# Kernel tuning notes

Measured on AMD Instinct MI355X. Metric: run time of the kernel, lower is better.

The kernel has to match this reference:

```python
import jax, jax.numpy as jnp
import numpy as np

ROPE_THETA = 10000.0


def _rope(x, pos, theta):
    # x: [B, H, S, d_k], pos: [S] int. Interleaved RoPE (pairs (2i, 2i+1)).
    d_k = x.shape[-1]
    inv_freq = theta ** (-2.0 * jnp.arange(d_k // 2, dtype=jnp.float32) / d_k)  # [d_k/2]
    ang = pos.astype(jnp.float32)[:, None] * inv_freq  # [S, d_k/2]
    cos, sin = jnp.cos(ang), jnp.sin(ang)
    xe, xo = x[..., 0::2], x[..., 1::2]
    re = xe * cos - xo * sin
    ro = xe * sin + xo * cos
    return jnp.stack([re, ro], axis=-1).reshape(x.shape)


def setup_inputs() -> dict:
    key = jax.random.key(0)
    ks = jax.random.split(key, 5)
    B, S, D = 2, 2048, 1024
    return {
        "in_features": jax.random.normal(ks[0], (B, S, D), jnp.float32),
        "q_proj_weight": jax.random.normal(ks[1], (D, D), jnp.float32) * (D ** -0.5),
        "k_proj_weight": jax.random.normal(ks[2], (D, D), jnp.float32) * (D ** -0.5),
        "v_proj_weight": jax.random.normal(ks[3], (D, D), jnp.float32) * (D ** -0.5),
        "o_proj_weight": jax.random.normal(ks[4], (D, D), jnp.float32) * (D ** -0.5),
        "token_positions": jnp.arange(S, dtype=jnp.int64),
        "d_model": 1024,
        "num_heads": 16,
    }


def reference(in_features, q_proj_weight, k_proj_weight, v_proj_weight,
              o_proj_weight, token_positions, d_model, num_heads):
    B, S, _ = in_features.shape
    d_k = d_model // num_heads

    def split_heads(x):  # [B, S, D] -> [B, H, S, d_k]
        return x.reshape(B, S, num_heads, d_k).transpose(0, 2, 1, 3)

    q = split_heads(in_features @ q_proj_weight.T)
    k = split_heads(in_features @ k_proj_weight.T)
    v = split_heads(in_features @ v_proj_weight.T)

    q = _rope(q, token_positions, ROPE_THETA)
    k = _rope(k, token_positions, ROPE_THETA)

    scores = jnp.einsum("bhqd,bhkd->bhqk", q, k) / jnp.sqrt(jnp.float32(d_k))
    causal = token_positions[:, None] >= token_positions[None, :]  # [S, S]
    scores = jnp.where(causal, scores, -jnp.inf)
    probs = jax.nn.softmax(scores, axis=-1)
    ctx = jnp.einsum("bhqk,bhkd->bhqd", probs, v)  # [B, H, S, d_k]
    ctx = ctx.transpose(0, 2, 1, 3).reshape(B, S, d_model)
    return ctx @ o_proj_weight.T
```

## Files before the change

kernel.cpp:

```cpp
#include <hip/hip_runtime.h>
#include <math.h>

typedef _Float16 f16;
typedef _Float16 f16x8 __attribute__((ext_vector_type(8)));
typedef float    f32x4 __attribute__((ext_vector_type(4)));

#define SEQ  2048
#define DM   1024
#define NH   16
#define DK   64
#define MTOT 4096

#define LOG2E 1.4426950408889634f

__global__ __launch_bounds__(256)
void cvt_all(const float* __restrict__ X,  const float* __restrict__ W0,
             const float* __restrict__ W1, const float* __restrict__ W2,
             const float* __restrict__ W3, f16* __restrict__ dst)
{
    const int i = (blockIdx.x * 256 + threadIdx.x) * 4;
    const float* src;
    if (i < (4 << 20)) {
        src = X + i;
    } else {
        const int j   = i - (4 << 20);
        const int sel = j >> 20;
        const float* W = (sel == 0) ? W0 : (sel == 1) ? W1 : (sel == 2) ? W2 : W3;
        src = W + (j & ((1 << 20) - 1));
    }
    float4 v = *(const float4*)src;
    f16 o[4] = {(f16)v.x, (f16)v.y, (f16)v.z, (f16)v.w};
    *(uint2*)&dst[i] = *(const uint2*)o;
}

__global__ __launch_bounds__(256)
void rope_table(float2* __restrict__ rt)
{
    const int i = blockIdx.x * 256 + threadIdx.x;
    const int s = i >> 5, p = i & 31;
    const float ang = (float)s * exp2f(-0.4152410118609203f * (float)p);
    float sn, cs;
    sincosf(ang, &sn, &cs);
    rt[i] = make_float2(cs, sn);
}

__global__ __launch_bounds__(512)
void gemm_qkv(const f16* __restrict__ A, const f16* __restrict__ W,
              f16* __restrict__ C, const float2* __restrict__ rt)
{
    __shared__ f16 As[128][72];
    __shared__ f16 Bs[128][72];

    const int tid  = threadIdx.x;
    const int wid  = tid >> 6, lane = tid & 63;
    const int l15  = lane & 15, l4 = lane >> 4;
    const int wm   = wid >> 2, wn = wid & 3;
    const int bm   = blockIdx.x * 128;
    const int sel  = blockIdx.y >> 3;
    const int bn   = (blockIdx.y & 7) * 128;
    const f16* B   = W + ((size_t)sel << 20);
    f16* Cb        = C + ((size_t)sel << 22);

    f32x4 acc[4][2];
    #pragma unroll
    for (int mi = 0; mi < 4; ++mi)
        #pragma unroll
        for (int ni = 0; ni < 2; ++ni)
            acc[mi][ni] = (f32x4){0.f, 0.f, 0.f, 0.f};

    for (int k0 = 0; k0 < DM; k0 += 64) {
        #pragma unroll
        for (int t = 0; t < 2; ++t) {
            const int li  = tid + t * 512;
            const int row = li >> 3, c8 = (li & 7) * 8;
            *(f16x8*)&As[row][c8] = *(const f16x8*)&A[(size_t)(bm + row) * DM + k0 + c8];
            *(f16x8*)&Bs[row][c8] = *(const f16x8*)&B[(size_t)(bn + row) * DM + k0 + c8];
        }
        __syncthreads();
        #pragma unroll
        for (int kc = 0; kc < 2; ++kc) {
            f16x8 af[4], bf[2];
            #pragma unroll
            for (int mi = 0; mi < 4; ++mi)
                af[mi] = *(const f16x8*)&As[wm*64 + mi*16 + l15][kc*32 + l4*8];
            #pragma unroll
            for (int ni = 0; ni < 2; ++ni)
                bf[ni] = *(const f16x8*)&Bs[wn*32 + ni*16 + l15][kc*32 + l4*8];
            #pragma unroll
            for (int mi = 0; mi < 4; ++mi)
                #pragma unroll
                for (int ni = 0; ni < 2; ++ni)
                    acc[mi][ni] = __builtin_amdgcn_mfma_f32_16x16x32_f16(
                        af[mi], bf[ni], acc[mi][ni], 0, 0, 0);
        }
        __syncthreads();
    }

    #pragma unroll
    for (int mi = 0; mi < 4; ++mi)
        #pragma unroll
        for (int ni = 0; ni < 2; ++ni)
            #pragma unroll
            for (int r = 0; r < 4; ++r) {
                const int row = bm + wm*64 + mi*16 + l4*4 + r;
                const int col = bn + wn*32 + ni*16 + l15;
                float v = acc[mi][ni][r];
                if (sel < 2) {
                    const float p   = __shfl_xor(v, 1);
                    const float2 cs = rt[((row & (SEQ-1)) << 5) | ((col & 63) >> 1)];
                    v = (col & 1) ? fmaf(v, cs.x,  p * cs.y)
                                  : fmaf(v, cs.x, -p * cs.y);
                }
                Cb[(size_t)row * DM + col] = (f16)v;
            }
}

__global__ __launch_bounds__(512)
void gemm_h(const f16* __restrict__ A, const f16* __restrict__ B,
            float* __restrict__ C)
{
    __shared__ f16 As[128][72];
    __shared__ f16 Bs[128][72];

    const int tid  = threadIdx.x;
    const int wid  = tid >> 6, lane = tid & 63;
    const int l15  = lane & 15, l4 = lane >> 4;
    const int wm   = wid >> 2, wn = wid & 3;
    const int bm   = blockIdx.x * 128, bn = blockIdx.y * 128;

    f32x4 acc[4][2];
    #pragma unroll
    for (int mi = 0; mi < 4; ++mi)
        #pragma unroll
        for (int ni = 0; ni < 2; ++ni)
            acc[mi][ni] = (f32x4){0.f, 0.f, 0.f, 0.f};

    for (int k0 = 0; k0 < DM; k0 += 64) {
        #pragma unroll
        for (int t = 0; t < 2; ++t) {
            const int li  = tid + t * 512;
            const int row = li >> 3, c8 = (li & 7) * 8;
            *(f16x8*)&As[row][c8] = *(const f16x8*)&A[(size_t)(bm + row) * DM + k0 + c8];
            *(f16x8*)&Bs[row][c8] = *(const f16x8*)&B[(size_t)(bn + row) * DM + k0 + c8];
        }
        __syncthreads();
        #pragma unroll
        for (int kc = 0; kc < 2; ++kc) {
            f16x8 af[4], bf[2];
            #pragma unroll
            for (int mi = 0; mi < 4; ++mi)
                af[mi] = *(const f16x8*)&As[wm*64 + mi*16 + l15][kc*32 + l4*8];
            #pragma unroll
            for (int ni = 0; ni < 2; ++ni)
                bf[ni] = *(const f16x8*)&Bs[wn*32 + ni*16 + l15][kc*32 + l4*8];
            #pragma unroll
            for (int mi = 0; mi < 4; ++mi)
                #pragma unroll
                for (int ni = 0; ni < 2; ++ni)
                    acc[mi][ni] = __builtin_amdgcn_mfma_f32_16x16x32_f16(
                        af[mi], bf[ni], acc[mi][ni], 0, 0, 0);
        }
        __syncthreads();
    }

    #pragma unroll
    for (int mi = 0; mi < 4; ++mi)
        #pragma unroll
        for (int ni = 0; ni < 2; ++ni)
            #pragma unroll
            for (int r = 0; r < 4; ++r) {
                const int row = bm + wm*64 + mi*16 + l4*4 + r;
                const int col = bn + wn*32 + ni*16 + l15;
                C[(size_t)row * DM + col] = acc[mi][ni][r];
            }
}

__global__ __launch_bounds__(512)
void flash_mfma(const f16* __restrict__ Q, const f16* __restrict__ K,
                const f16* __restrict__ V, f16* __restrict__ O)
{
    __shared__ f16 smem[6][64][72];

    const int bid = blockIdx.x;
    const int xcd = bid & 7, slot = bid >> 3;
    const int bh  = xcd * 4 + (slot >> 4);
    const int bx  = slot & 15;
    const int b   = bh >> 4, h = bh & 15;

    const int tid = threadIdx.x, wid = tid >> 6, lane = tid & 63;
    const int grp = wid >> 2, w4 = wid & 3;
    const int l15 = lane & 15, l4 = lane >> 4;
    const size_t base = ((size_t)b * SEQ) * DM + h * DK;

    f16 (*Ks)[72]  = smem[grp];
    f16 (*Vts)[72] = smem[2 + grp];
    f16 (*Ps)[72]  = smem[4 + grp];

    const int t256  = tid & 255;
    const int srow0 = t256 >> 3,        sc8 = (t256 & 7) * 8;
    const int srow1 = (t256 + 256) >> 3;
    const int spc0  = srow0 ^ ((t256 & 7) << 3);
    const int spc1  = srow1 ^ ((t256 & 7) << 3);

    f16x8 kreg[2], vreg[2];

    #pragma unroll 1
    for (int qsel = 0; qsel < 2; ++qsel) {
        const int qt     = qsel ? (31 - bx) : bx;
        const int ntiles = qt + 1;
        const int tmax   = (ntiles + 1) >> 1;

        f16x8 qf[2];
        {
            const size_t qrow = (size_t)(qt*64 + w4*16 + l15);
            #pragma unroll
            for (int kc = 0; kc < 2; ++kc) {
                qf[kc] = *(const f16x8*)&Q[base + qrow * DM + kc*32 + l4*8];
                #pragma unroll
                for (int j = 0; j < 8; ++j)
                    qf[kc][j] = (f16)((float)qf[kc][j] * (0.125f * LOG2E));
            }
        }

        float m_r[4], l_r[4];
        f32x4 acc_o[4];
        #pragma unroll
        for (int r = 0; r < 4; ++r) { m_r[r] = -INFINITY; l_r[r] = 0.f; }
        #pragma unroll
        for (int dg = 0; dg < 4; ++dg) acc_o[dg] = (f32x4){0.f, 0.f, 0.f, 0.f};

        if (grp < ntiles) {
            const size_t g0 = base + (size_t)(grp*64 + srow0) * DM + sc8;
            const size_t g1 = base + (size_t)(grp*64 + srow1) * DM + sc8;
            kreg[0] = *(const f16x8*)&K[g0]; vreg[0] = *(const f16x8*)&V[g0];
            kreg[1] = *(const f16x8*)&K[g1]; vreg[1] = *(const f16x8*)&V[g1];
        }
        __syncthreads();
        if (grp < ntiles) {
            *(f16x8*)&Ks[srow0][sc8] = kreg[0];
            *(f16x8*)&Ks[srow1][sc8] = kreg[1];
            #pragma unroll
            for (int j = 0; j < 8; ++j) { Vts[sc8+j][spc0] = vreg[0][j];
                                          Vts[sc8+j][spc1] = vreg[1][j]; }
        }
        __syncthreads();

        for (int t = 0; t < tmax; ++t) {
            const int  myt = 2*t + grp;
            const bool act = myt < ntiles;
            const int  nxt = myt + 2;

            if (nxt < ntiles) {
                const size_t g0 = base + (size_t)(nxt*64 + srow0) * DM + sc8;
                const size_t g1 = base + (size_t)(nxt*64 + srow1) * DM + sc8;
                kreg[0] = *(const f16x8*)&K[g0]; vreg[0] = *(const f16x8*)&V[g0];
                kreg[1] = *(const f16x8*)&K[g1]; vreg[1] = *(const f16x8*)&V[g1];
            }

            if (act) {
                f32x4 sc[4];
                #pragma unroll
                for (int cg = 0; cg < 4; ++cg) sc[cg] = (f32x4){0.f, 0.f, 0.f, 0.f};
                #pragma unroll
                for (int cg = 0; cg < 4; ++cg)
                    #pragma unroll
                    for (int kc = 0; kc < 2; ++kc) {
                        f16x8 bf = *(const f16x8*)&Ks[cg*16 + l15][kc*32 + l4*8];
                        sc[cg] = __builtin_amdgcn_mfma_f32_16x16x32_f16(qf[kc], bf, sc[cg], 0, 0, 0);
                    }

                if (myt == qt) {
                    #pragma unroll
                    for (int cg = 0; cg < 4; ++cg)
                        #pragma unroll
                        for (int r = 0; r < 4; ++r)
                            if (cg*16 + l15 > w4*16 + l4*4 + r) sc[cg][r] = -INFINITY;
                }

                #pragma unroll
                for (int r = 0; r < 4; ++r) {
                    float mx = fmaxf(fmaxf(sc[0][r], sc[1][r]), fmaxf(sc[2][r], sc[3][r]));
                    mx = fmaxf(mx, __shfl_xor(mx, 1));
                    mx = fmaxf(mx, __shfl_xor(mx, 2));
                    mx = fmaxf(mx, __shfl_xor(mx, 4));
                    mx = fmaxf(mx, __shfl_xor(mx, 8));
                    const float mn   = fmaxf(m_r[r], mx);
                    const float corr = exp2f(m_r[r] - mn);
                    float ps = 0.f;
                    #pragma unroll
                    for (int cg = 0; cg < 4; ++cg) {
                        const float pv = exp2f(sc[cg][r] - mn);
                        sc[cg][r] = pv;
                        ps += pv;
                    }
                    ps += __shfl_xor(ps, 1);
                    ps += __shfl_xor(ps, 2);
                    ps += __shfl_xor(ps, 4);
                    ps += __shfl_xor(ps, 8);
                    l_r[r] = l_r[r] * corr + ps;
                    m_r[r] = mn;
                    #pragma unroll
                    for (int dg = 0; dg < 4; ++dg) acc_o[dg][r] *= corr;
                }

                #pragma unroll
                for (int cg = 0; cg < 4; ++cg)
                    #pragma unroll
                    for (int r = 0; r < 4; ++r)
                        Ps[w4*16 + l4*4 + r][cg*16 + l15] = (f16)sc[cg][r];

                #pragma unroll
                for (int kc = 0; kc < 2; ++kc) {
                    f16x8 pa = *(const f16x8*)&Ps[w4*16 + l15][kc*32 + l4*8];
                    #pragma unroll
                    for (int dg = 0; dg < 4; ++dg) {
                        const int d   = dg*16 + l15;
                        const int pcr = (kc*32 + l4*8) ^ (((d >> 3) & 7) << 3);
                        f16x8 vb = *(const f16x8*)&Vts[d][pcr];
                        acc_o[dg] = __builtin_amdgcn_mfma_f32_16x16x32_f16(pa, vb, acc_o[dg], 0, 0, 0);
                    }
                }
            }

            __syncthreads();
            if (nxt < ntiles) {
                *(f16x8*)&Ks[srow0][sc8] = kreg[0];
                *(f16x8*)&Ks[srow1][sc8] = kreg[1];
                #pragma unroll
                for (int j = 0; j < 8; ++j) { Vts[sc8+j][spc0] = vreg[0][j];
                                              Vts[sc8+j][spc1] = vreg[1][j]; }
            }
            __syncthreads();
        }

        float* accx = (float*)&smem[0][0][0];
        float* mlx  = (float*)&smem[4][0][0];

        if (grp == 1) {
            #pragma unroll
            for (int r = 0; r < 4; ++r) {
                const int ql = w4*16 + l4*4 + r;
                mlx[ql]      = m_r[r];
                mlx[64 + ql] = l_r[r];
                #pragma unroll
                for (int dg = 0; dg < 4; ++dg)
                    accx[ql*64 + dg*16 + l15] = acc_o[dg][r];
            }
        }
        __syncthreads();
        if (grp == 0) {
            #pragma unroll
            for (int r = 0; r < 4; ++r) {
                const int ql = w4*16 + l4*4 + r;
                const float m1 = mlx[ql], l1 = mlx[64 + ql];
                const float m  = fmaxf(m_r[r], m1);
                const float c0 = exp2f(m_r[r] - m);
                const float c1 = exp2f(m1 - m);
                const float inv = 1.f / (l_r[r]*c0 + l1*c1);
                const size_t row = (size_t)(qt*64 + ql);
                #pragma unroll
                for (int dg = 0; dg < 4; ++dg) {
                    const float a1 = accx[ql*64 + dg*16 + l15];
                    O[base + row * DM + dg*16 + l15] =
                        (f16)((acc_o[dg][r]*c0 + a1*c1) * inv);
                }
            }
        }
    }
}

extern "C" void kernel_launch(void* const* d_in, const int* in_sizes, int n_in,
                              void* d_out, int out_size, void* d_ws, size_t ws_size,
                              hipStream_t stream)
{
    const float* X  = (const float*)d_in[0];
    const float* Wq = (const float*)d_in[1];
    const float* Wk = (const float*)d_in[2];
    const float* Wv = (const float*)d_in[3];
    const float* Wo = (const float*)d_in[4];

    f16* ws = (f16*)d_ws;
    const size_t M1 = 1u << 20;
    f16* Xh  = ws;
    f16* Wqh = ws + 4*M1;
    f16* Woh = ws + 7*M1;
    f16* Qh  = ws + 8*M1;
    f16* Kh  = ws + 12*M1;
    f16* Vh  = ws + 16*M1;
    f16* Ch  = ws + 20*M1;
    float2* rt = (float2*)(ws + 24*M1);

    cvt_all<<<8192, 256, 0, stream>>>(X, Wq, Wk, Wv, Wo, Xh);
    rope_table<<<256, 256, 0, stream>>>(rt);

    gemm_qkv<<<dim3(MTOT/128, 24), 512, 0, stream>>>(Xh, Wqh, Qh, rt);

    flash_mfma<<<512, 512, 0, stream>>>(Qh, Kh, Vh, Ch);

    gemm_h<<<dim3(MTOT/128, DM/128), 512, 0, stream>>>(Ch, Woh, (float*)d_out);
}
```

Baseline: 233.4 us.

## Use direct global-to-LDS loads and 4-wave 64x64 warp tiles in projection GEMMs

The two projection GEMMs now share one macro core. It stages A and B tiles with global_load_lds (direct global-to-LDS, bypassing VGPRs) using BK=32 and an unpadded LDS layout. Blocks are cut to 256 threads with 64x64 per-wave tiles (4x4 MFMAs), which raises operand reuse per LDS read. The risks are LDS bank conflicts from the unpadded 64-byte rows, twice as many barrier-separated k-steps, and no double buffering to hide load latency.

```diff
diff --git a/kernel.cpp b/kernel.cpp
--- a/kernel.cpp
+++ b/kernel.cpp
@@ -12,6 +12,13 @@
 #define MTOT 4096
 
 #define LOG2E 1.4426950408889634f
+
+__device__ __forceinline__ void gload16(const void* g, void* l)
+{
+    __builtin_amdgcn_global_load_lds(
+        (const __attribute__((address_space(1))) void*)g,
+        (__attribute__((address_space(3))) void*)l, 16, 0, 0);
+}
 
 __global__ __launch_bounds__(256)
 void cvt_all(const float* __restrict__ X,  const float* __restrict__ W0,
@@ -44,135 +51,82 @@
     rt[i] = make_float2(cs, sn);
 }
 
-__global__ __launch_bounds__(512)
+#define GEMM_CORE(EPILOG)                                                     \
+    __shared__ f16 As[128*32];                                                \
+    __shared__ f16 Bs[128*32];                                                \
+    const int tid = threadIdx.x;                                              \
+    const int wid = tid >> 6, lane = tid & 63;                                \
+    const int l15 = lane & 15, l4 = lane >> 4;                                \
+    const int wm  = wid >> 1, wn = wid & 1;                                   \
+    const int row0 = tid >> 2, col0 = (tid & 3) * 8;                          \
+    f32x4 acc[4][4];                                                          \
+    _Pragma("unroll")                                                         \
+    for (int mi = 0; mi < 4; ++mi)                                            \
+        _Pragma("unroll")                                                     \
+        for (int ni = 0; ni < 4; ++ni)                                        \
+            acc[mi][ni] = (f32x4){0.f, 0.f, 0.f, 0.f};                        \
+    for (int k0 = 0; k0 < DM; k0 += 32) {                                     \
+        gload16(&A[(size_t)(bm + row0)      * DM + k0 + col0], &As[tid*8]);   \
+        gload16(&A[(size_t)(bm + row0 + 64) * DM + k0 + col0], &As[(tid+256)*8]); \
+        gload16(&B[(size_t)(bn + row0)      * DM + k0 + col0], &Bs[tid*8]);   \
+        gload16(&B[(size_t)(bn + row0 + 64) * DM + k0 + col0], &Bs[(tid+256)*8]); \
+        __syncthreads();                                                      \
+        f16x8 af[4], bf[4];                                                   \
+        _Pragma("unroll")                                                     \
+        for (int mi = 0; mi < 4; ++mi)                                        \
+            af[mi] = *(const f16x8*)&As[(wm*64 + mi*16 + l15)*32 + l4*8];     \
+        _Pragma("unroll")                                                     \
+        for (int ni = 0; ni < 4; ++ni)                                        \
+            bf[ni] = *(const f16x8*)&Bs[(wn*64 + ni*16 + l15)*32 + l4*8];     \
+        _Pragma("unroll")                                                     \
+        for (int mi = 0; mi < 4; ++mi)                                        \
+            _Pragma("unroll")                                                 \
+            for (int ni = 0; ni < 4; ++ni)                                    \
+                acc[mi][ni] = __builtin_amdgcn_mfma_f32_16x16x32_f16(         \
+                    af[mi], bf[ni], acc[mi][ni], 0, 0, 0);                    \
+        __syncthreads();                                                      \
+    }                                                                         \
+    _Pragma("unroll")                                                         \
+    for (int mi = 0; mi < 4; ++mi)                                            \
+        _Pragma("unroll")                                                     \
+        for (int ni = 0; ni < 4; ++ni)                                        \
+            _Pragma("unroll")                                                 \
+            for (int r = 0; r < 4; ++r) {                                     \
+                const int row = bm + wm*64 + mi*16 + l4*4 + r;                \
+                const int col = bn + wn*64 + ni*16 + l15;                     \
+                float v = acc[mi][ni][r];                                     \
+                EPILOG                                                        \
+            }
+
+__global__ __launch_bounds__(256)
 void gemm_qkv(const f16* __restrict__ A, const f16* __restrict__ W,
               f16* __restrict__ C, const float2* __restrict__ rt)
 {
-    __shared__ f16 As[128][72];
-    __shared__ f16 Bs[128][72];
-
-    const int tid  = threadIdx.x;
-    const int wid  = tid >> 6, lane = tid & 63;
-    const int l15  = lane & 15, l4 = lane >> 4;
-    const int wm   = wid >> 2, wn = wid & 3;
-    const int bm   = blockIdx.x * 128;
-    const int sel  = blockIdx.y >> 3;
-    const int bn   = (blockIdx.y & 7) * 128;
-    const f16* B   = W + ((size_t)sel << 20);
-    f16* Cb        = C + ((size_t)sel << 22);
-
-    f32x4 acc[4][2];
-    #pragma unroll
-    for (int mi = 0; mi < 4; ++mi)
-        #pragma unroll
-        for (int ni = 0; ni < 2; ++ni)
-            acc[mi][ni] = (f32x4){0.f, 0.f, 0.f, 0.f};
-
-    for (int k0 = 0; k0 < DM; k0 += 64) {
-        #pragma unroll
-        for (int t = 0; t < 2; ++t) {
-            const int li  = tid + t * 512;
-            const int row = li >> 3, c8 = (li & 7) * 8;
-            *(f16x8*)&As[row][c8] = *(const f16x8*)&A[(size_t)(bm + row) * DM + k0 + c8];
-            *(f16x8*)&Bs[row][c8] = *(const f16x8*)&B[(size_t)(bn + row) * DM + k0 + c8];
-        }
-        __syncthreads();
-        #pragma unroll
-        for (int kc = 0; kc < 2; ++kc) {
-            f16x8 af[4], bf[2];
-            #pragma unroll
-            for (int mi = 0; mi < 4; ++mi)
-                af[mi] = *(const f16x8*)&As[wm*64 + mi*16 + l15][kc*32 + l4*8];
-            #pragma unroll
-            for (int ni = 0; ni < 2; ++ni)
-                bf[ni] = *(const f16x8*)&Bs[wn*32 + ni*16 + l15][kc*32 + l4*8];
-            #pragma unroll
-            for (int mi = 0; mi < 4; ++mi)
-                #pragma unroll
-                for (int ni = 0; ni < 2; ++ni)
-                    acc[mi][ni] = __builtin_amdgcn_mfma_f32_16x16x32_f16(
-                        af[mi], bf[ni], acc[mi][ni], 0, 0, 0);
-        }
-        __syncthreads();
-    }
-
-    #pragma unroll
-    for (int mi = 0; mi < 4; ++mi)
-        #pragma unroll
-        for (int ni = 0; ni < 2; ++ni)
-            #pragma unroll
-            for (int r = 0; r < 4; ++r) {
-                const int row = bm + wm*64 + mi*16 + l4*4 + r;
-                const int col = bn + wn*32 + ni*16 + l15;
-                float v = acc[mi][ni][r];
-                if (sel < 2) {
-                    const float p   = __shfl_xor(v, 1);
-                    const float2 cs = rt[((row & (SEQ-1)) << 5) | ((col & 63) >> 1)];
-                    v = (col & 1) ? fmaf(v, cs.x,  p * cs.y)
-                                  : fmaf(v, cs.x, -p * cs.y);
-                }
-                Cb[(size_t)row * DM + col] = (f16)v;
-            }
-}
-
-__global__ __launch_bounds__(512)
+    const int bm  = blockIdx.x * 128;
+    const int sel = blockIdx.y >> 3;
+    const int bn  = (blockIdx.y & 7) * 128;
+    const f16* B  = W + ((size_t)sel << 20);
+    f16* Cb       = C + ((size_t)sel << 22);
+
+    GEMM_CORE(
+        if (sel < 2) {
+            const float p   = __shfl_xor(v, 1);
+            const float2 cs = rt[((row & (SEQ-1)) << 5) | ((col & 63) >> 1)];
+            v = (col & 1) ? fmaf(v, cs.x,  p * cs.y)
+                          : fmaf(v, cs.x, -p * cs.y);
+        }
+        Cb[(size_t)row * DM + col] = (f16)v;
+    )
+}
+
+__global__ __launch_bounds__(256)
 void gemm_h(const f16* __restrict__ A, const f16* __restrict__ B,
             float* __restrict__ C)
 {
-    __shared__ f16 As[128][72];
-    __shared__ f16 Bs[128][72];
-
-    const int tid  = threadIdx.x;
-    const int wid  = tid >> 6, lane = tid & 63;
-    const int l15  = lane & 15, l4 = lane >> 4;
-    const int wm   = wid >> 2, wn = wid & 3;
-    const int bm   = blockIdx.x * 128, bn = blockIdx.y * 128;
-
-    f32x4 acc[4][2];
-    #pragma unroll
-    for (int mi = 0; mi < 4; ++mi)
-        #pragma unroll
-        for (int ni = 0; ni < 2; ++ni)
-            acc[mi][ni] = (f32x4){0.f, 0.f, 0.f, 0.f};
-
-    for (int k0 = 0; k0 < DM; k0 += 64) {
-        #pragma unroll
-        for (int t = 0; t < 2; ++t) {
-            const int li  = tid + t * 512;
-            const int row = li >> 3, c8 = (li & 7) * 8;
-            *(f16x8*)&As[row][c8] = *(const f16x8*)&A[(size_t)(bm + row) * DM + k0 + c8];
-            *(f16x8*)&Bs[row][c8] = *(const f16x8*)&B[(size_t)(bn + row) * DM + k0 + c8];
-        }
-        __syncthreads();
-        #pragma unroll
-        for (int kc = 0; kc < 2; ++kc) {
-            f16x8 af[4], bf[2];
-            #pragma unroll
-            for (int mi = 0; mi < 4; ++mi)
-                af[mi] = *(const f16x8*)&As[wm*64 + mi*16 + l15][kc*32 + l4*8];
-            #pragma unroll
-            for (int ni = 0; ni < 2; ++ni)
-                bf[ni] = *(const f16x8*)&Bs[wn*32 + ni*16 + l15][kc*32 + l4*8];
-            #pragma unroll
-            for (int mi = 0; mi < 4; ++mi)
-                #pragma unroll
-                for (int ni = 0; ni < 2; ++ni)
-                    acc[mi][ni] = __builtin_amdgcn_mfma_f32_16x16x32_f16(
-                        af[mi], bf[ni], acc[mi][ni], 0, 0, 0);
-        }
-        __syncthreads();
-    }
-
-    #pragma unroll
-    for (int mi = 0; mi < 4; ++mi)
-        #pragma unroll
-        for (int ni = 0; ni < 2; ++ni)
-            #pragma unroll
-            for (int r = 0; r < 4; ++r) {
-                const int row = bm + wm*64 + mi*16 + l4*4 + r;
-                const int col = bn + wn*32 + ni*16 + l15;
-                C[(size_t)row * DM + col] = acc[mi][ni][r];
-            }
+    const int bm = blockIdx.x * 128, bn = blockIdx.y * 128;
+    GEMM_CORE(
+        C[(size_t)row * DM + col] = v;
+    )
 }
 
 __global__ __launch_bounds__(512)
@@ -393,9 +347,9 @@
     cvt_all<<<8192, 256, 0, stream>>>(X, Wq, Wk, Wv, Wo, Xh);
     rope_table<<<256, 256, 0, stream>>>(rt);
 
-    gemm_qkv<<<dim3(MTOT/128, 24), 512, 0, stream>>>(Xh, Wqh, Qh, rt);
+    gemm_qkv<<<dim3(MTOT/128, 24), 256, 0, stream>>>(Xh, Wqh, Qh, rt);
 
     flash_mfma<<<512, 512, 0, stream>>>(Qh, Kh, Vh, Ch);
 
-    gemm_h<<<dim3(MTOT/128, DM/128), 512, 0, stream>>>(Ch, Woh, (float*)d_out);
-}
+    gemm_h<<<dim3(MTOT/128, DM/128), 256, 0, stream>>>(Ch, Woh, (float*)d_out);
+}
```

Result: slower. 262.4 us (+12.4%).
